# Kernel tuning notes

Measured on AMD Instinct MI355X. Metric: run time of the kernel, lower is better.

Reference implementation:

```python
import jax, jax.numpy as jnp
import numpy as np

HEADS = 8

def _layernorm(x, g, b, eps=1e-5):
    mu = x.mean(-1, keepdims=True)
    var = ((x - mu) ** 2).mean(-1, keepdims=True)
    return (x - mu) * jax.lax.rsqrt(var + eps) * g + b

def _four_region_attention(x, ln_g, ln_b, w_qkv, b_qkv, w_out, b_out):
    b, n, dim = x.shape
    W = int(np.sqrt(n))  # H == W, n = H*W
    xn = _layernorm(x, ln_g, ln_b)
    qkv = xn @ w_qkv + b_qkv  # [b, n, 3*inner]
    q, k, v = jnp.split(qkv, 3, axis=-1)
    split_heads = lambda t: t.reshape(b, n, HEADS, -1).transpose(0, 2, 1, 3)  # b h n d
    q, k, v = map(split_heads, (q, k, v))
    dh = q.shape[-1]
    scale = dh ** -0.5
    scores = jnp.einsum('bhqd,bhkd->bhqk', q, k) * scale  # [b, h, n, n]
    # region masks: query pos (h,w), key pos (i,j); to_qkv is position-wise
    # linear so per-region K/V recompute == slicing global K/V.
    row = jnp.arange(n) // W
    col = jnp.arange(n) % W
    le_r = row[None, :] <= row[:, None]  # i <= h
    ge_r = row[None, :] >= row[:, None]  # i >= h
    le_c = col[None, :] <= col[:, None]  # j <= w
    ge_c = col[None, :] >= col[:, None]  # j >= w
    masks = (le_r & le_c, le_r & ge_c, ge_r & le_c, ge_r & ge_c)
    neg = jnp.finfo(scores.dtype).min
    acc = jnp.zeros_like(q)
    for m in masks:  # all 4 regions are always non-empty (contain (h,w))
        attn = jax.nn.softmax(jnp.where(m, scores, neg), axis=-1)
        attn = jax.nn.relu(attn)  # identity on softmax output; kept for fidelity
        acc = acc + jnp.einsum('bhqk,bhkd->bhqd', attn, v)
    out = (acc / 4.0).transpose(0, 2, 1, 3).reshape(b, n, HEADS * dh)
    return out @ w_out + b_out

def setup_inputs() -> dict:
    key = jax.random.key(0)
    ks = jax.random.split(key, 3)
    b, n, dim = 8, 1024, 512
    dim_head = 64
    inner = HEADS * dim_head
    s = lambda fan: 1.0 / np.sqrt(fan)
    return {
        'x': jax.random.normal(ks[0], (b, n, dim), jnp.float32),
        'ln_g': jnp.ones((dim,), jnp.float32),
        'ln_b': jnp.zeros((dim,), jnp.float32),
        'w_qkv': jax.random.normal(ks[1], (dim, 3 * inner), jnp.float32) * s(dim),
        'b_qkv': jnp.zeros((3 * inner,), jnp.float32),
        'w_out': jax.random.normal(ks[2], (inner, dim), jnp.float32) * s(inner),
        'b_out': jnp.zeros((dim,), jnp.float32),
    }

def reference(x, ln_g, ln_b, w_qkv, b_qkv, w_out, b_out):
    return _four_region_attention(x, ln_g, ln_b, w_qkv, b_qkv, w_out, b_out)
```

## Files before the change

### kernel.cpp

```cpp
#include <hip/hip_runtime.h>
#include <hip/hip_bf16.h>

typedef unsigned short ushort_t;
typedef unsigned int uint32;
typedef __attribute__((ext_vector_type(8))) short short8;
typedef __attribute__((ext_vector_type(4))) float f32x4;
typedef __attribute__((ext_vector_type(16))) float f32x16;

#define BATCH 8
#define SEQ 1024
#define DIM 512
#define NHEADS 8
#define DH 64
#define NQKV 1536

__device__ __forceinline__ float bf2f(ushort_t u){ return __uint_as_float(((uint32)u) << 16); }
__device__ __forceinline__ ushort_t f2bf(float f){
  uint32 u = __float_as_uint(f);
  return (ushort_t)((u + 0x7fffu + ((u >> 16) & 1u)) >> 16);
}
__device__ __forceinline__ short8 ld8(const ushort_t* p){ return *reinterpret_cast<const short8*>(p); }
__device__ __forceinline__ f32x4 mfma16(short8 a, short8 b, f32x4 c){
  return __builtin_amdgcn_mfma_f32_16x16x32_bf16(a, b, c, 0, 0, 0);
}
__device__ __forceinline__ f32x16 mfma32(short8 a, short8 b, f32x16 c){
  return __builtin_amdgcn_mfma_f32_32x32x16_bf16(a, b, c, 0, 0, 0);
}
__device__ __forceinline__ void async16(const ushort_t* g, ushort_t* l){
  __builtin_amdgcn_global_load_lds((const __attribute__((address_space(1))) void*)g,
                                   (__attribute__((address_space(3))) void*)l, 16, 0, 0);
}
__device__ __forceinline__ uint32 cvtpk_bf16(float lo, float hi){
  uint32 d;
  asm("v_cvt_pk_bf16_f32 %0, %1, %2" : "=v"(d) : "v"(lo), "v"(hi));
  return d;
}
__device__ __forceinline__ void permswap32(uint32& a, uint32& b){
  asm volatile("v_permlane32_swap_b32 %0, %1" : "+v"(a), "+v"(b));
}
__device__ __forceinline__ short8 mk8(uint32 a, uint32 b, uint32 c, uint32 d){
  union { uint32 u[4]; short8 v; } t;
  t.u[0] = a; t.u[1] = b; t.u[2] = c; t.u[3] = d; return t.v;
}

__global__ __launch_bounds__(256) void prep_kernel(const float* __restrict__ x,
                                                   const float* __restrict__ g,
                                                   const float* __restrict__ bt,
                                                   ushort_t* __restrict__ xn,
                                                   const float* __restrict__ wqkv,
                                                   ushort_t* __restrict__ wqkvT,
                                                   const float* __restrict__ wout,
                                                   ushort_t* __restrict__ woutT){
  __shared__ float t[32][33];
  int bid = blockIdx.x;
  if (bid < 2048){
    int row  = bid * 4 + (threadIdx.x >> 6);
    int lane = threadIdx.x & 63;
    const float* xr = x + (size_t)row * DIM + lane * 8;
    float4 d0 = *reinterpret_cast<const float4*>(xr);
    float4 d1 = *reinterpret_cast<const float4*>(xr + 4);
    float v[8] = {d0.x, d0.y, d0.z, d0.w, d1.x, d1.y, d1.z, d1.w};
    float s = 0.f, ss = 0.f;
    #pragma unroll
    for (int i = 0; i < 8; i++){ s += v[i]; ss += v[i] * v[i]; }
    #pragma unroll
    for (int off = 1; off < 64; off <<= 1){ s += __shfl_xor(s, off); ss += __shfl_xor(ss, off); }
    float mean = s * (1.0f / DIM);
    float var  = ss * (1.0f / DIM) - mean * mean;
    float rstd = rsqrtf(fmaxf(var, 0.f) + 1e-5f);
    float4 g0 = *reinterpret_cast<const float4*>(g  + lane * 8);
    float4 g1 = *reinterpret_cast<const float4*>(g  + lane * 8 + 4);
    float4 b0 = *reinterpret_cast<const float4*>(bt + lane * 8);
    float4 b1 = *reinterpret_cast<const float4*>(bt + lane * 8 + 4);
    float gv[8] = {g0.x, g0.y, g0.z, g0.w, g1.x, g1.y, g1.z, g1.w};
    float bv[8] = {b0.x, b0.y, b0.z, b0.w, b1.x, b1.y, b1.z, b1.w};
    ushort_t o[8];
    #pragma unroll
    for (int i = 0; i < 8; i++) o[i] = f2bf((v[i] - mean) * rstd * gv[i] + bv[i]);
    uint4 od;
    od.x = o[0] | ((uint32)o[1] << 16); od.y = o[2] | ((uint32)o[3] << 16);
    od.z = o[4] | ((uint32)o[5] << 16); od.w = o[6] | ((uint32)o[7] << 16);
    *reinterpret_cast<uint4*>(xn + (size_t)row * DIM + lane * 8) = od;
  } else {
    const float* in; ushort_t* out; int R, C, bx, by;
    if (bid < 2816){ int b = bid - 2048; in = wqkv; out = wqkvT; R = 512; C = 1536; bx = b % 48; by = b / 48; }
    else           { int b = bid - 2816; in = wout; out = woutT; R = 512; C = 512;  bx = b % 16; by = b / 16; }
    int tx = threadIdx.x & 31, ty = threadIdx.x >> 5;
    int r0 = by * 32, c0 = bx * 32;
    #pragma unroll
    for (int i = 0; i < 4; i++) t[ty + 8*i][tx] = in[(size_t)(r0 + ty + 8*i) * C + c0 + tx];
    __syncthreads();
    #pragma unroll
    for (int i = 0; i < 4; i++) out[(size_t)(c0 + ty + 8*i) * R + r0 + tx] = f2bf(t[tx][ty + 8*i]);
  }
}

template<int MT>
__device__ __forceinline__ void gemm_core_t(const ushort_t* __restrict__ A,
                                            const ushort_t* __restrict__ Bt,
                                            int m0, int n0,
                                            ushort_t* ldsA, ushort_t* ldsB,
                                            f32x4 acc[MT][4]){
  int tid = threadIdx.x, w = tid >> 6, lane = tid & 63;
  int c16 = lane & 15, quad = lane >> 4;
  int r8 = lane >> 3, p8 = lane & 7;
  int srcChunk = p8 ^ r8;
  int w_row = w >> 1, w_col = w & 1;

  const ushort_t* ga[MT]; const ushort_t* gb[4];
  #pragma unroll
  for (int c = 0; c < MT; c++)
    ga[c] = A  + (size_t)(m0 + c * 32 + w * 8 + r8) * DIM + srcChunk * 8;
  #pragma unroll
  for (int c = 0; c < 4; c++)
    gb[c] = Bt + (size_t)(n0 + c * 32 + w * 8 + r8) * DIM + srcChunk * 8;
  #pragma unroll
  for (int mt = 0; mt < MT; mt++)
    #pragma unroll
    for (int nt = 0; nt < 4; nt++) acc[mt][nt] = (f32x4){0.f, 0.f, 0.f, 0.f};

  for (int it = 0; it < 8; it++){
    #pragma unroll
    for (int c = 0; c < MT; c++){ async16(ga[c], &ldsA[(c * 32 + w * 8) * 64]); ga[c] += 64; }
    #pragma unroll
    for (int c = 0; c < 4;  c++){ async16(gb[c], &ldsB[(c * 32 + w * 8) * 64]); gb[c] += 64; }
    __syncthreads();
    #pragma unroll
    for (int kk = 0; kk < 2; kk++){
      short8 af[MT], bfr[4];
      int phys = ((kk * 4 + quad) ^ (c16 & 7)) * 8;
      #pragma unroll
      for (int mt = 0; mt < MT; mt++)
        af[mt] = ld8(&ldsA[(w_row * (MT * 16) + mt * 16 + c16) * 64 + phys]);
      #pragma unroll
      for (int nt = 0; nt < 4; nt++)
        bfr[nt] = ld8(&ldsB[(w_col * 64 + nt * 16 + c16) * 64 + phys]);
      #pragma unroll
      for (int mt = 0; mt < MT; mt++)
        #pragma unroll
        for (int nt = 0; nt < 4; nt++)
          acc[mt][nt] = mfma16(af[mt], bfr[nt], acc[mt][nt]);
    }
    __syncthreads();
  }
}

__global__ __launch_bounds__(256) void qkv_gemm_kernel(const ushort_t* __restrict__ xn,
                                                       const ushort_t* __restrict__ wT,
                                                       const float* __restrict__ bias,
                                                       ushort_t* __restrict__ Qo,
                                                       ushort_t* __restrict__ Ko,
                                                       ushort_t* __restrict__ Vt){
  __shared__ __align__(16) ushort_t ldsA[64 * 64];
  __shared__ __align__(16) ushort_t ldsB[128 * 64];
  int m0 = blockIdx.x * 64, n0 = blockIdx.y * 128;
  f32x4 acc[2][4];
  gemm_core_t<2>(xn, wT, m0, n0, ldsA, ldsB, acc);

  int lane = threadIdx.x & 63, w = threadIdx.x >> 6;
  int c16 = lane & 15, quad = lane >> 4;
  int w_row = w >> 1, w_col = w & 1;
  int region = n0 >> 9;

  if (region < 2){
    float sc = (region == 0) ? 0.18033688011112042f : 1.0f;
    #pragma unroll
    for (int nt = 0; nt < 4; nt++){
      int col = n0 + w_col * 64 + nt * 16 + c16;
      float bv = bias[col];
      int cr = col & 511, h = cr >> 6, dd = cr & 63;
      #pragma unroll
      for (int mt = 0; mt < 2; mt++){
        #pragma unroll
        for (int r = 0; r < 4; r++){
          int row = m0 + w_row * 32 + mt * 16 + quad * 4 + r;
          int b = row >> 10, n = row & 1023;
          ushort_t o = f2bf((acc[mt][nt][r] + bv) * sc);
          if (region == 0){
            Qo[(((size_t)(b * NHEADS + h)) * SEQ + n) * DH + dd] = o;
          } else {
            Ko[((size_t)(b * NHEADS + h)) * SEQ * DH
               + (n >> 5) * 2048 + (dd >> 4) * 512 + ((dd >> 3) & 1) * 256
               + (n & 31) * 8 + (dd & 7)] = o;
          }
        }
      }
    }
  } else {
    #pragma unroll
    for (int nt = 0; nt < 4; nt++){
      int col = n0 + w_col * 64 + nt * 16 + c16;
      float bv = bias[col];
      int c2 = col - 1024; int h = c2 >> 6, dd = c2 & 63;
      #pragma unroll
      for (int mt = 0; mt < 2; mt++){
        int row0 = m0 + w_row * 32 + mt * 16 + quad * 4;
        int b = row0 >> 10, n = row0 & 1023;
        ushort_t o[4];
        #pragma unroll
        for (int r = 0; r < 4; r++) o[r] = f2bf(acc[mt][nt][r] + bv);
        uint2 val;
        val.x = o[0] | ((uint32)o[1] << 16);
        val.y = o[2] | ((uint32)o[3] << 16);
        *reinterpret_cast<uint2*>(Vt + (((size_t)(b * NHEADS + h)) * 128 + (n >> 3)) * 512
                                  + dd * 8 + (n & 7)) = val;
      }
    }
  }
}

__global__ __launch_bounds__(256) void out_gemm_kernel(const ushort_t* __restrict__ ctx,
                                                       const ushort_t* __restrict__ wT,
                                                       const float* __restrict__ bias,
                                                       float* __restrict__ out){
  __shared__ __align__(16) ushort_t ldsA[32 * 64];
  __shared__ __align__(16) ushort_t ldsB[128 * 64];
  int m0 = blockIdx.x * 32, n0 = blockIdx.y * 128;
  f32x4 acc[1][4];
  gemm_core_t<1>(ctx, wT, m0, n0, ldsA, ldsB, acc);

  int lane = threadIdx.x & 63, w = threadIdx.x >> 6;
  int c16 = lane & 15, quad = lane >> 4;
  int w_row = w >> 1, w_col = w & 1;
  #pragma unroll
  for (int nt = 0; nt < 4; nt++){
    int col = n0 + w_col * 64 + nt * 16 + c16;
    float bv = bias[col];
    #pragma unroll
    for (int r = 0; r < 4; r++){
      int row = m0 + w_row * 16 + quad * 4 + r;
      out[(size_t)row * DIM + col] = acc[0][nt][r] + bv;
    }
  }
}

__global__ __launch_bounds__(256, 2) void attn_kernel(const ushort_t* __restrict__ Qg,
                                                      const ushort_t* __restrict__ Kg,
                                                      const ushort_t* __restrict__ Vtg,
                                                      ushort_t* __restrict__ ctx){
  int bh = blockIdx.x;
  int wv = threadIdx.x >> 6, lane = threadIdx.x & 63;
  int qt = blockIdx.y * 4 + wv;
  int w  = lane & 31;
  int hi = lane >> 5;
  int hq = qt;

  const ushort_t* Qh = Qg  + (size_t)bh * SEQ * DH;
  const ushort_t* Kh = Kg  + (size_t)bh * SEQ * DH;
  const ushort_t* Vh = Vtg + (size_t)bh * SEQ * DH;

  short8 qf[4];
  {
    const ushort_t* qp = Qh + (size_t)(qt * 32 + w) * DH + hi * 8;
    #pragma unroll
    for (int f = 0; f < 4; f++) qf[f] = ld8(qp + f * 16);
  }
  const ushort_t* kp = Kh + (size_t)lane * 8;

  float mle[16], mge[16];
  #pragma unroll
  for (int r = 0; r < 16; r++){
    int jr = (r & 3) + 8 * (r >> 2) + 4 * hi;
    mle[r] = (jr <= w) ? 1.f : 0.f;
    mge[r] = (jr >= w) ? 1.f : 0.f;
  }

  auto qk = [&](const short8* kf) -> f32x16 {
    f32x16 s;
    #pragma unroll
    for (int r = 0; r < 16; r++) s[r] = 0.f;
    #pragma unroll
    for (int f = 0; f < 4; f++) s = mfma32(kf[f], qf[f], s);
    return s;
  };

  float tle = 0.f, tge = 0.f, ble = 0.f, bge = 0.f;
  auto p1 = [&](const short8* kf, int i){
    f32x16 s = qk(kf);
    float a0 = 0.f, a1 = 0.f, g0 = 0.f, g1 = 0.f;
    #pragma unroll
    for (int r = 0; r < 16; r++){
      float e = __builtin_amdgcn_exp2f(s[r]);
      if (r & 1){ a1 = fmaf(mle[r], e, a1); g1 = fmaf(mge[r], e, g1); }
      else      { a0 = fmaf(mle[r], e, a0); g0 = fmaf(mge[r], e, g0); }
    }
    float sle = a0 + a1, sge = g0 + g1;
    if (i <= hq){ tle += sle; tge += sge; }
    if (i >= hq){ ble += sle; bge += sge; }
  };
  {
    short8 kA[4], kB[4];
    #pragma unroll
    for (int f = 0; f < 4; f++) kA[f] = ld8(kp + f * 512);
    for (int i = 0; i < 32; i += 2){
      #pragma unroll
      for (int f = 0; f < 4; f++) kB[f] = ld8(kp + (size_t)(i + 1) * 2048 + f * 512);
      p1(kA, i);
      int nx = (i + 2) & 31;
      #pragma unroll
      for (int f = 0; f < 4; f++) kA[f] = ld8(kp + (size_t)nx * 2048 + f * 512);
      p1(kB, i + 1);
    }
  }
  tle += __shfl_xor(tle, 32); tge += __shfl_xor(tge, 32);
  ble += __shfl_xor(ble, 32); bge += __shfl_xor(bge, 32);
  float i1 = 0.25f / fmaxf(tle, 1e-30f);
  float i2 = 0.25f / fmaxf(tge, 1e-30f);
  float i3 = 0.25f / fmaxf(ble, 1e-30f);
  float i4 = 0.25f / fmaxf(bge, 1e-30f);

  float wcur[16], wbt[16];
  #pragma unroll
  for (int r = 0; r < 16; r++){
    wcur[r] = fmaf(i1, mle[r], i2 * mge[r]);
    wbt[r]  = fmaf(i3, mle[r], i4 * mge[r]);
  }

  f32x16 accLo, accHi;
  #pragma unroll
  for (int r = 0; r < 16; r++){ accLo[r] = 0.f; accHi[r] = 0.f; }
  const ushort_t* vbase = Vh + (size_t)hi * 512 + (size_t)w * 8;

  auto p2 = [&](const short8* kf, int i){
    short8 vl0 = ld8(vbase + (size_t)i * 2048);
    short8 vl1 = ld8(vbase + (size_t)i * 2048 + 1024);
    short8 vh0 = ld8(vbase + (size_t)i * 2048 + 256);
    short8 vh1 = ld8(vbase + (size_t)i * 2048 + 1280);
    f32x16 s = qk(kf);
    if (i == hq){
      #pragma unroll
      for (int r = 0; r < 16; r++) wcur[r] += wbt[r];
    } else if (i == hq + 1){
      #pragma unroll
      for (int r = 0; r < 16; r++) wcur[r] = wbt[r];
    }
    float P[16];
    #pragma unroll
    for (int r = 0; r < 16; r++) P[r] = __builtin_amdgcn_exp2f(s[r]) * wcur[r];
    uint32 x0 = cvtpk_bf16(P[0],  P[1]);
    uint32 x1 = cvtpk_bf16(P[2],  P[3]);
    uint32 y0 = cvtpk_bf16(P[4],  P[5]);
    uint32 y1 = cvtpk_bf16(P[6],  P[7]);
    uint32 x2 = cvtpk_bf16(P[8],  P[9]);
    uint32 x3 = cvtpk_bf16(P[10], P[11]);
    uint32 y2 = cvtpk_bf16(P[12], P[13]);
    uint32 y3 = cvtpk_bf16(P[14], P[15]);
    permswap32(x0, y0);
    permswap32(x1, y1);
    permswap32(x2, y2);
    permswap32(x3, y3);
    short8 fa0 = mk8(x0, x1, y0, y1);
    short8 fa1 = mk8(x2, x3, y2, y3);
    accLo = mfma32(fa0, vl0, accLo);
    accLo = mfma32(fa1, vl1, accLo);
    accHi = mfma32(fa0, vh0, accHi);
    accHi = mfma32(fa1, vh1, accHi);
  };
  {
    short8 kA[4], kB[4];
    #pragma unroll
    for (int f = 0; f < 4; f++) kA[f] = ld8(kp + f * 512);
    for (int i = 0; i < 32; i += 2){
      #pragma unroll
      for (int f = 0; f < 4; f++) kB[f] = ld8(kp + (size_t)(i + 1) * 2048 + f * 512);
      p2(kA, i);
      int nx = (i + 2) & 31;
      #pragma unroll
      for (int f = 0; f < 4; f++) kA[f] = ld8(kp + (size_t)nx * 2048 + f * 512);
      p2(kB, i + 1);
    }
  }

  int bidx = bh >> 3, h = bh & 7;
  size_t obase = ((size_t)(bidx * SEQ + qt * 32)) * DIM + h * DH + w;
  #pragma unroll
  for (int r = 0; r < 16; r++){
    int qrow = (r & 3) + 8 * (r >> 2) + 4 * hi;
    ctx[obase + (size_t)qrow * DIM]      = f2bf(accLo[r]);
    ctx[obase + (size_t)qrow * DIM + 32] = f2bf(accHi[r]);
  }
}

extern "C" void kernel_launch(void* const* d_in, const int* in_sizes, int n_in,
                              void* d_out, int out_size, void* d_ws, size_t ws_size,
                              hipStream_t stream){
  (void)in_sizes; (void)n_in; (void)out_size; (void)ws_size;
  const float* x    = (const float*)d_in[0];
  const float* ln_g = (const float*)d_in[1];
  const float* ln_b = (const float*)d_in[2];
  const float* wqkv = (const float*)d_in[3];
  const float* bqkv = (const float*)d_in[4];
  const float* wout = (const float*)d_in[5];
  const float* bout = (const float*)d_in[6];
  float* out = (float*)d_out;

  char* ws = (char*)d_ws;
  ushort_t* xn    = (ushort_t*)(ws);
  ushort_t* ctx   = (ushort_t*)(ws);
  ushort_t* wqkvT = (ushort_t*)(ws + 8388608);
  ushort_t* woutT = (ushort_t*)(ws + 9961472);
  ushort_t* Qb    = (ushort_t*)(ws + 10485760);
  ushort_t* Kb    = (ushort_t*)(ws + 18874368);
  ushort_t* Vtb   = (ushort_t*)(ws + 27262976);

  hipLaunchKernelGGL(prep_kernel,     dim3(3072),    dim3(256), 0, stream,
                     x, ln_g, ln_b, xn, wqkv, wqkvT, wout, woutT);
  hipLaunchKernelGGL(qkv_gemm_kernel, dim3(128, 12), dim3(256), 0, stream, xn, wqkvT, bqkv, Qb, Kb, Vtb);
  hipLaunchKernelGGL(attn_kernel,     dim3(64, 8),   dim3(256), 0, stream, Qb, Kb, Vtb, ctx);
  hipLaunchKernelGGL(out_gemm_kernel, dim3(256, 4),  dim3(256), 0, stream, ctx, woutT, bout, out);
}
```

Measured before the change: 148.3 us.

## Split attention key range across wave pairs and enlarge QKV GEMM tiles

The attention kernel now assigns two waves to each 32-query tile. Each wave sums softmax denominators over half the key blocks, and the two halves are combined through shared memory with a block barrier. In the second pass each wave computes only half of the head dimension of the output, which halves its accumulator registers and doubles the grid. The QKV GEMM tile grows from 64 to 128 rows per block to improve operand reuse, at the cost of fewer blocks and more registers. The attention split adds a sync, repeats the QK^T score computation in both waves of a pair during the second pass, and runs under an explicit waves-per-EU occupancy target.

```diff
diff --git a/kernel.cpp b/kernel.cpp
--- a/kernel.cpp
+++ b/kernel.cpp
@@ -151,11 +151,11 @@
                                                        ushort_t* __restrict__ Qo,
                                                        ushort_t* __restrict__ Ko,
                                                        ushort_t* __restrict__ Vt){
-  __shared__ __align__(16) ushort_t ldsA[64 * 64];
+  __shared__ __align__(16) ushort_t ldsA[128 * 64];
   __shared__ __align__(16) ushort_t ldsB[128 * 64];
-  int m0 = blockIdx.x * 64, n0 = blockIdx.y * 128;
-  f32x4 acc[2][4];
-  gemm_core_t<2>(xn, wT, m0, n0, ldsA, ldsB, acc);
+  int m0 = blockIdx.x * 128, n0 = blockIdx.y * 128;
+  f32x4 acc[4][4];
+  gemm_core_t<4>(xn, wT, m0, n0, ldsA, ldsB, acc);
 
   int lane = threadIdx.x & 63, w = threadIdx.x >> 6;
   int c16 = lane & 15, quad = lane >> 4;
@@ -170,10 +170,10 @@
       float bv = bias[col];
       int cr = col & 511, h = cr >> 6, dd = cr & 63;
       #pragma unroll
-      for (int mt = 0; mt < 2; mt++){
+      for (int mt = 0; mt < 4; mt++){
         #pragma unroll
         for (int r = 0; r < 4; r++){
-          int row = m0 + w_row * 32 + mt * 16 + quad * 4 + r;
+          int row = m0 + w_row * 64 + mt * 16 + quad * 4 + r;
           int b = row >> 10, n = row & 1023;
           ushort_t o = f2bf((acc[mt][nt][r] + bv) * sc);
           if (region == 0){
@@ -193,8 +193,8 @@
       float bv = bias[col];
       int c2 = col - 1024; int h = c2 >> 6, dd = c2 & 63;
       #pragma unroll
-      for (int mt = 0; mt < 2; mt++){
-        int row0 = m0 + w_row * 32 + mt * 16 + quad * 4;
+      for (int mt = 0; mt < 4; mt++){
+        int row0 = m0 + w_row * 64 + mt * 16 + quad * 4;
         int b = row0 >> 10, n = row0 & 1023;
         ushort_t o[4];
         #pragma unroll
@@ -234,16 +234,21 @@
   }
 }
 
-__global__ __launch_bounds__(256, 2) void attn_kernel(const ushort_t* __restrict__ Qg,
-                                                      const ushort_t* __restrict__ Kg,
-                                                      const ushort_t* __restrict__ Vtg,
-                                                      ushort_t* __restrict__ ctx){
+__global__ __launch_bounds__(256) __attribute__((amdgpu_waves_per_eu(4, 4)))
+void attn_kernel(const ushort_t* __restrict__ Qg,
+                 const ushort_t* __restrict__ Kg,
+                 const ushort_t* __restrict__ Vtg,
+                 ushort_t* __restrict__ ctx){
+  __shared__ float sdn[2][2][32][4];
+
   int bh = blockIdx.x;
   int wv = threadIdx.x >> 6, lane = threadIdx.x & 63;
-  int qt = blockIdx.y * 4 + wv;
+  int qsel = wv >> 1, dsel = wv & 1;
+  int qt = blockIdx.y * 2 + qsel;
   int w  = lane & 31;
   int hi = lane >> 5;
   int hq = qt;
+  int i0 = dsel << 4;
 
   const ushort_t* Qh = Qg  + (size_t)bh * SEQ * DH;
   const ushort_t* Kh = Kg  + (size_t)bh * SEQ * DH;
@@ -291,12 +296,13 @@
   {
     short8 kA[4], kB[4];
     #pragma unroll
-    for (int f = 0; f < 4; f++) kA[f] = ld8(kp + f * 512);
-    for (int i = 0; i < 32; i += 2){
+    for (int f = 0; f < 4; f++) kA[f] = ld8(kp + (size_t)i0 * 2048 + f * 512);
+    for (int ii = 0; ii < 16; ii += 2){
+      int i = i0 + ii;
       #pragma unroll
       for (int f = 0; f < 4; f++) kB[f] = ld8(kp + (size_t)(i + 1) * 2048 + f * 512);
       p1(kA, i);
-      int nx = (i + 2) & 31;
+      int nx = i0 + ((ii + 2) & 15);
       #pragma unroll
       for (int f = 0; f < 4; f++) kA[f] = ld8(kp + (size_t)nx * 2048 + f * 512);
       p1(kB, i + 1);
@@ -304,6 +310,15 @@
   }
   tle += __shfl_xor(tle, 32); tge += __shfl_xor(tge, 32);
   ble += __shfl_xor(ble, 32); bge += __shfl_xor(bge, 32);
+  if (lane < 32){
+    float4 d4 = {tle, tge, ble, bge};
+    *reinterpret_cast<float4*>(&sdn[qsel][dsel][w][0]) = d4;
+  }
+  __syncthreads();
+  {
+    float4 o4 = *reinterpret_cast<const float4*>(&sdn[qsel][1 - dsel][w][0]);
+    tle += o4.x; tge += o4.y; ble += o4.z; bge += o4.w;
+  }
   float i1 = 0.25f / fmaxf(tle, 1e-30f);
   float i2 = 0.25f / fmaxf(tge, 1e-30f);
   float i3 = 0.25f / fmaxf(ble, 1e-30f);
@@ -316,16 +331,14 @@
     wbt[r]  = fmaf(i3, mle[r], i4 * mge[r]);
   }
 
-  f32x16 accLo, accHi;
-  #pragma unroll
-  for (int r = 0; r < 16; r++){ accLo[r] = 0.f; accHi[r] = 0.f; }
-  const ushort_t* vbase = Vh + (size_t)hi * 512 + (size_t)w * 8;
+  f32x16 acc;
+  #pragma unroll
+  for (int r = 0; r < 16; r++) acc[r] = 0.f;
+  const ushort_t* vbase = Vh + (size_t)hi * 512 + (size_t)w * 8 + dsel * 256;
 
   auto p2 = [&](const short8* kf, int i){
-    short8 vl0 = ld8(vbase + (size_t)i * 2048);
-    short8 vl1 = ld8(vbase + (size_t)i * 2048 + 1024);
-    short8 vh0 = ld8(vbase + (size_t)i * 2048 + 256);
-    short8 vh1 = ld8(vbase + (size_t)i * 2048 + 1280);
+    short8 v0 = ld8(vbase + (size_t)i * 2048);
+    short8 v1 = ld8(vbase + (size_t)i * 2048 + 1024);
     f32x16 s = qk(kf);
     if (i == hq){
       #pragma unroll
@@ -351,10 +364,8 @@
     permswap32(x3, y3);
     short8 fa0 = mk8(x0, x1, y0, y1);
     short8 fa1 = mk8(x2, x3, y2, y3);
-    accLo = mfma32(fa0, vl0, accLo);
-    accLo = mfma32(fa1, vl1, accLo);
-    accHi = mfma32(fa0, vh0, accHi);
-    accHi = mfma32(fa1, vh1, accHi);
+    acc = mfma32(fa0, v0, acc);
+    acc = mfma32(fa1, v1, acc);
   };
   {
     short8 kA[4], kB[4];
@@ -372,12 +383,11 @@
   }
 
   int bidx = bh >> 3, h = bh & 7;
-  size_t obase = ((size_t)(bidx * SEQ + qt * 32)) * DIM + h * DH + w;
+  size_t obase = ((size_t)(bidx * SEQ + qt * 32)) * DIM + h * DH + dsel * 32 + w;
   #pragma unroll
   for (int r = 0; r < 16; r++){
     int qrow = (r & 3) + 8 * (r >> 2) + 4 * hi;
-    ctx[obase + (size_t)qrow * DIM]      = f2bf(accLo[r]);
-    ctx[obase + (size_t)qrow * DIM + 32] = f2bf(accHi[r]);
+    ctx[obase + (size_t)qrow * DIM] = f2bf(acc[r]);
   }
 }
 
@@ -405,7 +415,7 @@
 
   hipLaunchKernelGGL(prep_kernel,     dim3(3072),    dim3(256), 0, stream,
                      x, ln_g, ln_b, xn, wqkv, wqkvT, wout, woutT);
-  hipLaunchKernelGGL(qkv_gemm_kernel, dim3(128, 12), dim3(256), 0, stream, xn, wqkvT, bqkv, Qb, Kb, Vtb);
-  hipLaunchKernelGGL(attn_kernel,     dim3(64, 8),   dim3(256), 0, stream, Qb, Kb, Vtb, ctx);
+  hipLaunchKernelGGL(qkv_gemm_kernel, dim3(64, 12),  dim3(256), 0, stream, xn, wqkvT, bqkv, Qb, Kb, Vtb);
+  hipLaunchKernelGGL(attn_kernel,     dim3(64, 16),  dim3(256), 0, stream, Qb, Kb, Vtb, ctx);
   hipLaunchKernelGGL(out_gemm_kernel, dim3(256, 4),  dim3(256), 0, stream, ctx, woutT, bout, out);
 }
```

Result: slower. 261.5 us (+76.3%).

## Stage K tiles in shared LDS and fold region weights into MFMA accumulator

Applied to the files above, without the earlier changes.

The attention kernel now copies each head's K into a 64KB LDS buffer in two halves using async copies, so the four waves of a block share one copy instead of each wave streaming K from global memory. The two K passes are reordered so the half already resident in LDS is reused across the pass boundary. The per-region softmax weights are also folded in as log2 values used as the initial accumulator of the QK MFMA, which removes a per-element multiply after exp2. In exchange, the K loads are no longer overlapped with compute, and the block must wait at barriers while K is restaged. The larger LDS footprint can also lower occupancy.

```diff
diff --git a/kernel.cpp b/kernel.cpp
--- a/kernel.cpp
+++ b/kernel.cpp
@@ -238,6 +238,8 @@
                                                       const ushort_t* __restrict__ Kg,
                                                       const ushort_t* __restrict__ Vtg,
                                                       ushort_t* __restrict__ ctx){
+  __shared__ __align__(16) ushort_t ldsK[16 * 2048];
+
   int bh = blockIdx.x;
   int wv = threadIdx.x >> 6, lane = threadIdx.x & 63;
   int qt = blockIdx.y * 4 + wv;
@@ -249,13 +251,22 @@
   const ushort_t* Kh = Kg  + (size_t)bh * SEQ * DH;
   const ushort_t* Vh = Vtg + (size_t)bh * SEQ * DH;
 
+  auto stageK = [&](int half){
+    const ushort_t* ks = Kh + (size_t)half * 32768 + (size_t)wv * 8192 + (size_t)lane * 8;
+    ushort_t* ld = ldsK + wv * 8192;
+    #pragma unroll
+    for (int k = 0; k < 16; k++)
+      async16(ks + k * 512, ld + k * 512);
+  };
+
+  stageK(1);
+
   short8 qf[4];
   {
     const ushort_t* qp = Qh + (size_t)(qt * 32 + w) * DH + hi * 8;
     #pragma unroll
     for (int f = 0; f < 4; f++) qf[f] = ld8(qp + f * 16);
   }
-  const ushort_t* kp = Kh + (size_t)lane * 8;
 
   float mle[16], mge[16];
   #pragma unroll
@@ -265,43 +276,43 @@
     mge[r] = (jr >= w) ? 1.f : 0.f;
   }
 
-  auto qk = [&](const short8* kf) -> f32x16 {
-    f32x16 s;
-    #pragma unroll
-    for (int r = 0; r < 16; r++) s[r] = 0.f;
-    #pragma unroll
-    for (int f = 0; f < 4; f++) s = mfma32(kf[f], qf[f], s);
-    return s;
+  __syncthreads();
+
+  const ushort_t* klane = ldsK + lane * 8;
+
+  float tle = 0.f, tge = 0.f, ble = 0.f, bge = 0.f;
+  auto p1half = [&](int s){
+    for (int ii = 0; ii < 16; ii++){
+      int i = s + ii;
+      short8 k0 = ld8(klane + ii * 2048);
+      short8 k1 = ld8(klane + ii * 2048 + 512);
+      short8 k2 = ld8(klane + ii * 2048 + 1024);
+      short8 k3 = ld8(klane + ii * 2048 + 1536);
+      f32x16 sv;
+      #pragma unroll
+      for (int r = 0; r < 16; r++) sv[r] = 0.f;
+      sv = mfma32(k0, qf[0], sv);
+      sv = mfma32(k1, qf[1], sv);
+      sv = mfma32(k2, qf[2], sv);
+      sv = mfma32(k3, qf[3], sv);
+      float a0 = 0.f, a1 = 0.f, g0 = 0.f, g1 = 0.f;
+      #pragma unroll
+      for (int r = 0; r < 16; r++){
+        float e = __builtin_amdgcn_exp2f(sv[r]);
+        if (r & 1){ a1 = fmaf(mle[r], e, a1); g1 = fmaf(mge[r], e, g1); }
+        else      { a0 = fmaf(mle[r], e, a0); g0 = fmaf(mge[r], e, g0); }
+      }
+      float sle = a0 + a1, sge = g0 + g1;
+      if (i <= hq){ tle += sle; tge += sge; }
+      if (i >= hq){ ble += sle; bge += sge; }
+    }
   };
-
-  float tle = 0.f, tge = 0.f, ble = 0.f, bge = 0.f;
-  auto p1 = [&](const short8* kf, int i){
-    f32x16 s = qk(kf);
-    float a0 = 0.f, a1 = 0.f, g0 = 0.f, g1 = 0.f;
-    #pragma unroll
-    for (int r = 0; r < 16; r++){
-      float e = __builtin_amdgcn_exp2f(s[r]);
-      if (r & 1){ a1 = fmaf(mle[r], e, a1); g1 = fmaf(mge[r], e, g1); }
-      else      { a0 = fmaf(mle[r], e, a0); g0 = fmaf(mge[r], e, g0); }
-    }
-    float sle = a0 + a1, sge = g0 + g1;
-    if (i <= hq){ tle += sle; tge += sge; }
-    if (i >= hq){ ble += sle; bge += sge; }
-  };
-  {
-    short8 kA[4], kB[4];
-    #pragma unroll
-    for (int f = 0; f < 4; f++) kA[f] = ld8(kp + f * 512);
-    for (int i = 0; i < 32; i += 2){
-      #pragma unroll
-      for (int f = 0; f < 4; f++) kB[f] = ld8(kp + (size_t)(i + 1) * 2048 + f * 512);
-      p1(kA, i);
-      int nx = (i + 2) & 31;
-      #pragma unroll
-      for (int f = 0; f < 4; f++) kA[f] = ld8(kp + (size_t)nx * 2048 + f * 512);
-      p1(kB, i + 1);
-    }
-  }
+  p1half(16);
+  __syncthreads();
+  stageK(0);
+  __syncthreads();
+  p1half(0);
+
   tle += __shfl_xor(tle, 32); tge += __shfl_xor(tge, 32);
   ble += __shfl_xor(ble, 32); bge += __shfl_xor(bge, 32);
   float i1 = 0.25f / fmaxf(tle, 1e-30f);
@@ -309,67 +320,77 @@
   float i3 = 0.25f / fmaxf(ble, 1e-30f);
   float i4 = 0.25f / fmaxf(bge, 1e-30f);
 
-  float wcur[16], wbt[16];
+  float wa[16], wbt[16];
   #pragma unroll
   for (int r = 0; r < 16; r++){
-    wcur[r] = fmaf(i1, mle[r], i2 * mge[r]);
-    wbt[r]  = fmaf(i3, mle[r], i4 * mge[r]);
+    wa[r]  = fmaf(i1, mle[r], i2 * mge[r]);
+    wbt[r] = fmaf(i3, mle[r], i4 * mge[r]);
   }
 
   f32x16 accLo, accHi;
   #pragma unroll
   for (int r = 0; r < 16; r++){ accLo[r] = 0.f; accHi[r] = 0.f; }
   const ushort_t* vbase = Vh + (size_t)hi * 512 + (size_t)w * 8;
-
-  auto p2 = [&](const short8* kf, int i){
-    short8 vl0 = ld8(vbase + (size_t)i * 2048);
-    short8 vl1 = ld8(vbase + (size_t)i * 2048 + 1024);
-    short8 vh0 = ld8(vbase + (size_t)i * 2048 + 256);
-    short8 vh1 = ld8(vbase + (size_t)i * 2048 + 1280);
-    f32x16 s = qk(kf);
-    if (i == hq){
-      #pragma unroll
-      for (int r = 0; r < 16; r++) wcur[r] += wbt[r];
-    } else if (i == hq + 1){
-      #pragma unroll
-      for (int r = 0; r < 16; r++) wcur[r] = wbt[r];
-    }
-    float P[16];
-    #pragma unroll
-    for (int r = 0; r < 16; r++) P[r] = __builtin_amdgcn_exp2f(s[r]) * wcur[r];
-    uint32 x0 = cvtpk_bf16(P[0],  P[1]);
-    uint32 x1 = cvtpk_bf16(P[2],  P[3]);
-    uint32 y0 = cvtpk_bf16(P[4],  P[5]);
-    uint32 y1 = cvtpk_bf16(P[6],  P[7]);
-    uint32 x2 = cvtpk_bf16(P[8],  P[9]);
-    uint32 x3 = cvtpk_bf16(P[10], P[11]);
-    uint32 y2 = cvtpk_bf16(P[12], P[13]);
-    uint32 y3 = cvtpk_bf16(P[14], P[15]);
-    permswap32(x0, y0);
-    permswap32(x1, y1);
-    permswap32(x2, y2);
-    permswap32(x3, y3);
-    short8 fa0 = mk8(x0, x1, y0, y1);
-    short8 fa1 = mk8(x2, x3, y2, y3);
-    accLo = mfma32(fa0, vl0, accLo);
-    accLo = mfma32(fa1, vl1, accLo);
-    accHi = mfma32(fa0, vh0, accHi);
-    accHi = mfma32(fa1, vh1, accHi);
+  f32x16 lw;
+
+  auto p2half = [&](int s){
+    #pragma unroll
+    for (int r = 0; r < 16; r++){
+      float w0 = (s < hq) ? wa[r] : ((s == hq) ? wa[r] + wbt[r] : wbt[r]);
+      lw[r] = __builtin_amdgcn_logf(w0);
+    }
+    for (int ii = 0; ii < 16; ii++){
+      int i = s + ii;
+      short8 vl0 = ld8(vbase + (size_t)i * 2048);
+      short8 vl1 = ld8(vbase + (size_t)i * 2048 + 1024);
+      short8 vh0 = ld8(vbase + (size_t)i * 2048 + 256);
+      short8 vh1 = ld8(vbase + (size_t)i * 2048 + 1280);
+      if (ii > 0){
+        if (i == hq){
+          #pragma unroll
+          for (int r = 0; r < 16; r++) lw[r] = __builtin_amdgcn_logf(wa[r] + wbt[r]);
+        } else if (i == hq + 1){
+          #pragma unroll
+          for (int r = 0; r < 16; r++) lw[r] = __builtin_amdgcn_logf(wbt[r]);
+        }
+      }
+      short8 k0 = ld8(klane + ii * 2048);
+      short8 k1 = ld8(klane + ii * 2048 + 512);
+      short8 k2 = ld8(klane + ii * 2048 + 1024);
+      short8 k3 = ld8(klane + ii * 2048 + 1536);
+      f32x16 sv = mfma32(k0, qf[0], lw);
+      sv = mfma32(k1, qf[1], sv);
+      sv = mfma32(k2, qf[2], sv);
+      sv = mfma32(k3, qf[3], sv);
+      float P[16];
+      #pragma unroll
+      for (int r = 0; r < 16; r++) P[r] = __builtin_amdgcn_exp2f(sv[r]);
+      uint32 x0 = cvtpk_bf16(P[0],  P[1]);
+      uint32 x1 = cvtpk_bf16(P[2],  P[3]);
+      uint32 y0 = cvtpk_bf16(P[4],  P[5]);
+      uint32 y1 = cvtpk_bf16(P[6],  P[7]);
+      uint32 x2 = cvtpk_bf16(P[8],  P[9]);
+      uint32 x3 = cvtpk_bf16(P[10], P[11]);
+      uint32 y2 = cvtpk_bf16(P[12], P[13]);
+      uint32 y3 = cvtpk_bf16(P[14], P[15]);
+      permswap32(x0, y0);
+      permswap32(x1, y1);
+      permswap32(x2, y2);
+      permswap32(x3, y3);
+      short8 fa0 = mk8(x0, x1, y0, y1);
+      short8 fa1 = mk8(x2, x3, y2, y3);
+      accLo = mfma32(fa0, vl0, accLo);
+      accLo = mfma32(fa1, vl1, accLo);
+      accHi = mfma32(fa0, vh0, accHi);
+      accHi = mfma32(fa1, vh1, accHi);
+    }
   };
-  {
-    short8 kA[4], kB[4];
-    #pragma unroll
-    for (int f = 0; f < 4; f++) kA[f] = ld8(kp + f * 512);
-    for (int i = 0; i < 32; i += 2){
-      #pragma unroll
-      for (int f = 0; f < 4; f++) kB[f] = ld8(kp + (size_t)(i + 1) * 2048 + f * 512);
-      p2(kA, i);
-      int nx = (i + 2) & 31;
-      #pragma unroll
-      for (int f = 0; f < 4; f++) kA[f] = ld8(kp + (size_t)nx * 2048 + f * 512);
-      p2(kB, i + 1);
-    }
-  }
+
+  p2half(0);
+  __syncthreads();
+  stageK(1);
+  __syncthreads();
+  p2half(16);
 
   int bidx = bh >> 3, h = bh & 7;
   size_t obase = ((size_t)(bidx * SEQ + qt * 32)) * DIM + h * DH + w;
```

After: 185.7 us. 25.2% more time.

## Fuse two-pass region attention into single pass with four unnormalized accumulators

Applied to the files above, without the earlier changes.

Replaces the two-pass scheme (first pass computes the four region denominators, second pass recomputes QK and exp to build weighted P·V) with one pass that keeps four separate unnormalized P·V accumulators (top/bottom × le/ge) and normalizes them at the end through a shared-memory exchange of per-row denominators. This removes the duplicated QK MFMAs, exp evaluations and K loads. In exchange it raises the P·V MFMA count per tile (two masked P fragments, up to four accumulator sets), adds eight 16-wide accumulator vectors of register pressure that may hurt occupancy at launch_bounds(256,2), and drops the explicit double-buffered K prefetch.

```diff
diff --git a/kernel.cpp b/kernel.cpp
--- a/kernel.cpp
+++ b/kernel.cpp
@@ -238,6 +238,8 @@
                                                       const ushort_t* __restrict__ Kg,
                                                       const ushort_t* __restrict__ Vtg,
                                                       ushort_t* __restrict__ ctx){
+  __shared__ float sdn[4][32][4];
+
   int bh = blockIdx.x;
   int wv = threadIdx.x >> 6, lane = threadIdx.x & 63;
   int qt = blockIdx.y * 4 + wv;
@@ -265,43 +267,80 @@
     mge[r] = (jr >= w) ? 1.f : 0.f;
   }
 
-  auto qk = [&](const short8* kf) -> f32x16 {
+  f32x16 aTleL, aTgeL, aBleL, aBgeL, aTleH, aTgeH, aBleH, aBgeH;
+  #pragma unroll
+  for (int r = 0; r < 16; r++){
+    aTleL[r] = 0.f; aTgeL[r] = 0.f; aBleL[r] = 0.f; aBgeL[r] = 0.f;
+    aTleH[r] = 0.f; aTgeH[r] = 0.f; aBleH[r] = 0.f; aBgeH[r] = 0.f;
+  }
+  float tle = 0.f, tge = 0.f, ble = 0.f, bge = 0.f;
+  const ushort_t* vbase = Vh + (size_t)hi * 512 + (size_t)w * 8;
+
+  for (int i = 0; i < 32; i++){
+    short8 k0 = ld8(kp + (size_t)i * 2048);
+    short8 k1 = ld8(kp + (size_t)i * 2048 + 512);
+    short8 k2 = ld8(kp + (size_t)i * 2048 + 1024);
+    short8 k3 = ld8(kp + (size_t)i * 2048 + 1536);
+    short8 vl0 = ld8(vbase + (size_t)i * 2048);
+    short8 vl1 = ld8(vbase + (size_t)i * 2048 + 1024);
+    short8 vh0 = ld8(vbase + (size_t)i * 2048 + 256);
+    short8 vh1 = ld8(vbase + (size_t)i * 2048 + 1280);
     f32x16 s;
     #pragma unroll
     for (int r = 0; r < 16; r++) s[r] = 0.f;
-    #pragma unroll
-    for (int f = 0; f < 4; f++) s = mfma32(kf[f], qf[f], s);
-    return s;
-  };
-
-  float tle = 0.f, tge = 0.f, ble = 0.f, bge = 0.f;
-  auto p1 = [&](const short8* kf, int i){
-    f32x16 s = qk(kf);
+    s = mfma32(k0, qf[0], s);
+    s = mfma32(k1, qf[1], s);
+    s = mfma32(k2, qf[2], s);
+    s = mfma32(k3, qf[3], s);
+    float e[16];
     float a0 = 0.f, a1 = 0.f, g0 = 0.f, g1 = 0.f;
     #pragma unroll
     for (int r = 0; r < 16; r++){
-      float e = __builtin_amdgcn_exp2f(s[r]);
-      if (r & 1){ a1 = fmaf(mle[r], e, a1); g1 = fmaf(mge[r], e, g1); }
-      else      { a0 = fmaf(mle[r], e, a0); g0 = fmaf(mge[r], e, g0); }
+      e[r] = __builtin_amdgcn_exp2f(s[r]);
+      if (r & 1){ a1 = fmaf(mle[r], e[r], a1); g1 = fmaf(mge[r], e[r], g1); }
+      else      { a0 = fmaf(mle[r], e[r], a0); g0 = fmaf(mge[r], e[r], g0); }
     }
     float sle = a0 + a1, sge = g0 + g1;
-    if (i <= hq){ tle += sle; tge += sge; }
-    if (i >= hq){ ble += sle; bge += sge; }
-  };
-  {
-    short8 kA[4], kB[4];
-    #pragma unroll
-    for (int f = 0; f < 4; f++) kA[f] = ld8(kp + f * 512);
-    for (int i = 0; i < 32; i += 2){
-      #pragma unroll
-      for (int f = 0; f < 4; f++) kB[f] = ld8(kp + (size_t)(i + 1) * 2048 + f * 512);
-      p1(kA, i);
-      int nx = (i + 2) & 31;
-      #pragma unroll
-      for (int f = 0; f < 4; f++) kA[f] = ld8(kp + (size_t)nx * 2048 + f * 512);
-      p1(kB, i + 1);
-    }
-  }
+    uint32 lx0 = cvtpk_bf16(e[0]*mle[0],   e[1]*mle[1]);
+    uint32 lx1 = cvtpk_bf16(e[2]*mle[2],   e[3]*mle[3]);
+    uint32 ly0 = cvtpk_bf16(e[4]*mle[4],   e[5]*mle[5]);
+    uint32 ly1 = cvtpk_bf16(e[6]*mle[6],   e[7]*mle[7]);
+    uint32 lx2 = cvtpk_bf16(e[8]*mle[8],   e[9]*mle[9]);
+    uint32 lx3 = cvtpk_bf16(e[10]*mle[10], e[11]*mle[11]);
+    uint32 ly2 = cvtpk_bf16(e[12]*mle[12], e[13]*mle[13]);
+    uint32 ly3 = cvtpk_bf16(e[14]*mle[14], e[15]*mle[15]);
+    permswap32(lx0, ly0); permswap32(lx1, ly1);
+    permswap32(lx2, ly2); permswap32(lx3, ly3);
+    short8 fle0 = mk8(lx0, lx1, ly0, ly1);
+    short8 fle1 = mk8(lx2, lx3, ly2, ly3);
+    uint32 gx0 = cvtpk_bf16(e[0]*mge[0],   e[1]*mge[1]);
+    uint32 gx1 = cvtpk_bf16(e[2]*mge[2],   e[3]*mge[3]);
+    uint32 gy0 = cvtpk_bf16(e[4]*mge[4],   e[5]*mge[5]);
+    uint32 gy1 = cvtpk_bf16(e[6]*mge[6],   e[7]*mge[7]);
+    uint32 gx2 = cvtpk_bf16(e[8]*mge[8],   e[9]*mge[9]);
+    uint32 gx3 = cvtpk_bf16(e[10]*mge[10], e[11]*mge[11]);
+    uint32 gy2 = cvtpk_bf16(e[12]*mge[12], e[13]*mge[13]);
+    uint32 gy3 = cvtpk_bf16(e[14]*mge[14], e[15]*mge[15]);
+    permswap32(gx0, gy0); permswap32(gx1, gy1);
+    permswap32(gx2, gy2); permswap32(gx3, gy3);
+    short8 fge0 = mk8(gx0, gx1, gy0, gy1);
+    short8 fge1 = mk8(gx2, gx3, gy2, gy3);
+    if (i <= hq){
+      tle += sle; tge += sge;
+      aTleL = mfma32(fle0, vl0, aTleL); aTleL = mfma32(fle1, vl1, aTleL);
+      aTleH = mfma32(fle0, vh0, aTleH); aTleH = mfma32(fle1, vh1, aTleH);
+      aTgeL = mfma32(fge0, vl0, aTgeL); aTgeL = mfma32(fge1, vl1, aTgeL);
+      aTgeH = mfma32(fge0, vh0, aTgeH); aTgeH = mfma32(fge1, vh1, aTgeH);
+    }
+    if (i >= hq){
+      ble += sle; bge += sge;
+      aBleL = mfma32(fle0, vl0, aBleL); aBleL = mfma32(fle1, vl1, aBleL);
+      aBleH = mfma32(fle0, vh0, aBleH); aBleH = mfma32(fle1, vh1, aBleH);
+      aBgeL = mfma32(fge0, vl0, aBgeL); aBgeL = mfma32(fge1, vl1, aBgeL);
+      aBgeH = mfma32(fge0, vh0, aBgeH); aBgeH = mfma32(fge1, vh1, aBgeH);
+    }
+  }
+
   tle += __shfl_xor(tle, 32); tge += __shfl_xor(tge, 32);
   ble += __shfl_xor(ble, 32); bge += __shfl_xor(bge, 32);
   float i1 = 0.25f / fmaxf(tle, 1e-30f);
@@ -309,75 +348,22 @@
   float i3 = 0.25f / fmaxf(ble, 1e-30f);
   float i4 = 0.25f / fmaxf(bge, 1e-30f);
 
-  float wcur[16], wbt[16];
-  #pragma unroll
-  for (int r = 0; r < 16; r++){
-    wcur[r] = fmaf(i1, mle[r], i2 * mge[r]);
-    wbt[r]  = fmaf(i3, mle[r], i4 * mge[r]);
-  }
-
-  f32x16 accLo, accHi;
-  #pragma unroll
-  for (int r = 0; r < 16; r++){ accLo[r] = 0.f; accHi[r] = 0.f; }
-  const ushort_t* vbase = Vh + (size_t)hi * 512 + (size_t)w * 8;
-
-  auto p2 = [&](const short8* kf, int i){
-    short8 vl0 = ld8(vbase + (size_t)i * 2048);
-    short8 vl1 = ld8(vbase + (size_t)i * 2048 + 1024);
-    short8 vh0 = ld8(vbase + (size_t)i * 2048 + 256);
-    short8 vh1 = ld8(vbase + (size_t)i * 2048 + 1280);
-    f32x16 s = qk(kf);
-    if (i == hq){
-      #pragma unroll
-      for (int r = 0; r < 16; r++) wcur[r] += wbt[r];
-    } else if (i == hq + 1){
-      #pragma unroll
-      for (int r = 0; r < 16; r++) wcur[r] = wbt[r];
-    }
-    float P[16];
-    #pragma unroll
-    for (int r = 0; r < 16; r++) P[r] = __builtin_amdgcn_exp2f(s[r]) * wcur[r];
-    uint32 x0 = cvtpk_bf16(P[0],  P[1]);
-    uint32 x1 = cvtpk_bf16(P[2],  P[3]);
-    uint32 y0 = cvtpk_bf16(P[4],  P[5]);
-    uint32 y1 = cvtpk_bf16(P[6],  P[7]);
-    uint32 x2 = cvtpk_bf16(P[8],  P[9]);
-    uint32 x3 = cvtpk_bf16(P[10], P[11]);
-    uint32 y2 = cvtpk_bf16(P[12], P[13]);
-    uint32 y3 = cvtpk_bf16(P[14], P[15]);
-    permswap32(x0, y0);
-    permswap32(x1, y1);
-    permswap32(x2, y2);
-    permswap32(x3, y3);
-    short8 fa0 = mk8(x0, x1, y0, y1);
-    short8 fa1 = mk8(x2, x3, y2, y3);
-    accLo = mfma32(fa0, vl0, accLo);
-    accLo = mfma32(fa1, vl1, accLo);
-    accHi = mfma32(fa0, vh0, accHi);
-    accHi = mfma32(fa1, vh1, accHi);
-  };
-  {
-    short8 kA[4], kB[4];
-    #pragma unroll
-    for (int f = 0; f < 4; f++) kA[f] = ld8(kp + f * 512);
-    for (int i = 0; i < 32; i += 2){
-      #pragma unroll
-      for (int f = 0; f < 4; f++) kB[f] = ld8(kp + (size_t)(i + 1) * 2048 + f * 512);
-      p2(kA, i);
-      int nx = (i + 2) & 31;
-      #pragma unroll
-      for (int f = 0; f < 4; f++) kA[f] = ld8(kp + (size_t)nx * 2048 + f * 512);
-      p2(kB, i + 1);
-    }
-  }
+  if (lane < 32){
+    float4 d4 = {i1, i2, i3, i4};
+    *reinterpret_cast<float4*>(&sdn[wv][w][0]) = d4;
+  }
+  __syncthreads();
 
   int bidx = bh >> 3, h = bh & 7;
   size_t obase = ((size_t)(bidx * SEQ + qt * 32)) * DIM + h * DH + w;
   #pragma unroll
   for (int r = 0; r < 16; r++){
     int qrow = (r & 3) + 8 * (r >> 2) + 4 * hi;
-    ctx[obase + (size_t)qrow * DIM]      = f2bf(accLo[r]);
-    ctx[obase + (size_t)qrow * DIM + 32] = f2bf(accHi[r]);
+    float4 dn = *reinterpret_cast<const float4*>(&sdn[wv][qrow][0]);
+    float oL = dn.x * aTleL[r] + dn.y * aTgeL[r] + dn.z * aBleL[r] + dn.w * aBgeL[r];
+    float oH = dn.x * aTleH[r] + dn.y * aTgeH[r] + dn.z * aBleH[r] + dn.w * aBgeH[r];
+    ctx[obase + (size_t)qrow * DIM]      = f2bf(oL);
+    ctx[obase + (size_t)qrow * DIM + 32] = f2bf(oH);
   }
 }
 
```

Result: faster. 142.7 us, median of 2 (-3.8%).
